# Optimization experiments

Measured on AMD Instinct MI355X. Metric: run time of the kernel, lower is better.

## Reference

```python
import jax, jax.numpy as jnp
import numpy as np

N_NODES = 20000
N_EDGES = 400000
DIM = 128       # dim
NB = 16         # radial basis size
ZD = 16         # species encoding dim
N_SPECIES = 51
CUTOFF = 5.0
NLAYERS = 2
N_ONSITE = 3


def radial_basis(r):
    # 'gaussian_rinv': gaussians placed uniformly in inverse-distance space (HIP-NN style)
    rinv = 1.0 / r
    mus = jnp.linspace(1.0 / CUTOFF, 1.0, NB, dtype=r.dtype)
    sigma = mus[1] - mus[0]
    return jnp.exp(-0.5 * ((rinv[:, None] - mus[None, :]) / sigma) ** 2)  # [E, NB]


def setup_inputs() -> dict:
    key = jax.random.key(0)
    ks = jax.random.split(key, 16)
    species = jax.random.randint(ks[0], (N_NODES,), 1, N_SPECIES)
    edge_src = jax.random.randint(ks[1], (N_EDGES,), 0, N_NODES)
    edge_dst = jax.random.randint(ks[2], (N_EDGES,), 0, N_NODES)
    distances = jax.random.uniform(ks[3], (N_EDGES,), minval=0.8, maxval=CUTOFF)
    switch = jax.random.uniform(ks[4], (N_EDGES,))
    Z = jax.random.normal(ks[5], (N_SPECIES, ZD))  # species encoding table
    Ws0 = jax.random.normal(ks[6], (ZD, DIM)) / np.sqrt(ZD)
    bs0 = jnp.zeros((DIM,), jnp.float32)
    V0 = jax.random.normal(ks[7], (NB, ZD, DIM)) / np.sqrt(NB * ZD)
    Ws1 = jax.random.normal(ks[8], (DIM, DIM)) / np.sqrt(DIM)
    bs1 = jnp.zeros((DIM,), jnp.float32)
    V1 = jax.random.normal(ks[9], (NB, DIM, DIM)) / np.sqrt(NB * DIM)
    Won_a = jax.random.normal(ks[10], (NLAYERS, N_ONSITE, DIM, DIM)) / np.sqrt(DIM)
    bon_a = jnp.zeros((NLAYERS, N_ONSITE, DIM), jnp.float32)
    Won_b = jax.random.normal(ks[11], (NLAYERS, N_ONSITE, DIM, DIM)) / np.sqrt(DIM)
    bon_b = jnp.zeros((NLAYERS, N_ONSITE, DIM), jnp.float32)
    return dict(species=species, edge_src=edge_src, edge_dst=edge_dst,
                distances=distances, switch=switch, Z=Z,
                Ws0=Ws0, bs0=bs0, V0=V0, Ws1=Ws1, bs1=bs1, V1=V1,
                Won_a=Won_a, bon_a=bon_a, Won_b=Won_b, bon_b=bon_b)


def reference(species, edge_src, edge_dst, distances, switch, Z,
              Ws0, bs0, V0, Ws1, bs1, V1, Won_a, bon_a, Won_b, bon_b):
    zi = Z[species]                       # [N, ZD] species encoding
    s = radial_basis(distances)           # [E, NB] (identical basis each layer)
    sw = switch[:, None]                  # [E, 1]
    Ws, bs, Vs = (Ws0, Ws1), (bs0, bs1), (V0, V1)
    zis = []
    for layer in range(NLAYERS):
        zself = zi @ Ws[layer] + bs[layer]                        # [N, DIM]
        # mij = einsum('ej,ek,jkl->el', s, zi[edge_dst], V): per-edge outer then one GEMM
        zdst = zi[edge_dst]                                       # [E, k] gather
        outer = s[:, :, None] * zdst[:, None, :]                  # [E, NB, k]
        mij = outer.reshape(outer.shape[0], -1) @ Vs[layer].reshape(-1, DIM)  # [E, DIM]
        zi = jax.nn.silu(zself.at[edge_src].add(mij * sw))        # scatter-add
        for j in range(N_ONSITE):                                 # residual 2-layer MLPs
            h = jax.nn.silu(zi @ Won_a[layer, j] + bon_a[layer, j])
            zi = zi + h @ Won_b[layer, j] + bon_b[layer, j]
        zis.append(zi)
    # (embedding, embedding_layers)
    return zi, jnp.stack(zis, axis=1)
```

## Files before the change

kernel.cpp:

```cpp
#include <hip/hip_runtime.h>
#include <stdint.h>

#define NNODES 20000
#define NEDGES 400000
#define MTILES 1250
#define MT2    625
#define KS1 68

typedef __attribute__((ext_vector_type(8))) short short8;
typedef __attribute__((ext_vector_type(4))) float floatx4;

__device__ __forceinline__ float bf2f(uint16_t u){ return __uint_as_float(((uint32_t)u)<<16); }
__device__ __forceinline__ uint16_t f2bf(float f){
  uint32_t x = __float_as_uint(f);
  x += 0x7FFFu + ((x>>16)&1u);
  return (uint16_t)(x>>16);
}
__device__ __forceinline__ uint32_t packbf(float a, float b){
  return (uint32_t)f2bf(a) | ((uint32_t)f2bf(b)<<16);
}
__device__ __forceinline__ float siluf(float x){ return x/(1.0f+__expf(-x)); }
__device__ __forceinline__ float ldf(const void* p, int i, int md){
  return (md==1) ? bf2f(((const uint16_t*)p)[i]) : ((const float*)p)[i];
}

#define OFF_V0   0
#define N_V0     32768
#define OFF_WS1  32768
#define N_WS1    16384
#define OFF_BS1  49152
#define N_BS1    128
#define OFF_V1   49280
#define N_V1     262144
#define OFF_WA   311424
#define N_WA     98304
#define OFF_BA   409728
#define N_BA     768
#define OFF_WB   410496
#define N_WB     98304
#define OFF_BB   508800
#define N_BB     768
#define N_CONV   509568

__global__ void k_probe(const void* dist, int* mode){
  if(threadIdx.x != 0 || blockIdx.x != 0) return;
  const float* f = (const float*)dist;
  const uint16_t* h = (const uint16_t*)dist;
  int okf = 1, okb = 1;
  for(int i=0;i<256;i++){
    float a = f[i];       okf &= (a >= 0.7f) & (a <= 5.1f);
    float b = bf2f(h[i]); okb &= (b >= 0.7f) & (b <= 5.1f);
  }
  *mode = okb ? 1 : (okf ? 0 : 1);
}

__global__ __launch_bounds__(256) void k_conv(const void* s0,const void* s1,const void* s2,const void* s3,
                                              const void* s4,const void* s5,const void* s6,const void* s7,
                                              const int* __restrict__ modep, float* __restrict__ dst){
  int md = *modep;
  int i = blockIdx.x*256 + threadIdx.x;
  if(i >= N_CONV) return;
  const void* src; int t = i;
  if(t < N_V0){src=s0;}
  else if((t-=N_V0) < N_WS1){src=s1;}
  else if((t-=N_WS1) < N_BS1){src=s2;}
  else if((t-=N_BS1) < N_V1){src=s3;}
  else if((t-=N_V1) < N_WA){src=s4;}
  else if((t-=N_WA) < N_BA){src=s5;}
  else if((t-=N_BA) < N_WB){src=s6;}
  else {t-=N_WB; src=s7;}
  dst[i] = ldf(src, t, md);
}

__global__ __launch_bounds__(256) void k_hist(const int* __restrict__ src, int* __restrict__ cnt){
  int e = blockIdx.x*256 + threadIdx.x;
  if(e < NEDGES){
    int s = src[e];
    if((unsigned)s < NNODES) atomicAdd(&cnt[s], 1);
  }
}

__global__ __launch_bounds__(1024) void k_scan(int* cnt_cur, int* offs){
  __shared__ int wsum[16];
  int t = threadIdx.x;
  const int chunk = (NNODES + 1023)/1024;
  int lo = t*chunk, hi = lo+chunk;
  if(lo > NNODES) lo = NNODES;
  if(hi > NNODES) hi = NNODES;
  int s = 0;
  for(int i=lo;i<hi;i++) s += cnt_cur[i];
  int lane = t&63, wv = t>>6;
  int v = s;
  #pragma unroll
  for(int d=1; d<64; d<<=1){
    int u = __shfl_up(v, d);
    if(lane >= d) v += u;
  }
  if(lane==63) wsum[wv] = v;
  __syncthreads();
  if(t==0){
    int run = 0;
    #pragma unroll
    for(int i=0;i<16;i++){ int c = wsum[i]; wsum[i] = run; run += c; }
  }
  __syncthreads();
  int run = wsum[wv] + (v - s);
  for(int i=lo;i<hi;i++){
    int c = cnt_cur[i];
    offs[i] = run;
    cnt_cur[i] = run;
    run += c;
  }
  if(t==1023) offs[NNODES] = run;
}

__global__ __launch_bounds__(256) void k_fillG(const int* __restrict__ src,
                                               const int* __restrict__ edst,
                                               const int* __restrict__ species,
                                               int* __restrict__ cur,
                                               const void* __restrict__ dist,
                                               const void* __restrict__ sw,
                                               const int* __restrict__ modep,
                                               int* __restrict__ dsts,
                                               int* __restrict__ sps,
                                               uint16_t* __restrict__ gs){
  int e = blockIdx.x*256 + threadIdx.x;
  if(e >= NEDGES) return;
  int md = *modep;
  int s = src[e];
  if((unsigned)s >= NNODES) s = 0;
  int p = atomicAdd(&cur[s], 1);
  if((unsigned)p >= NEDGES) p = 0;
  int dn = edst[e];
  if((unsigned)dn >= NNODES) dn = 0;
  dsts[p] = dn;
  int sp = species[dn];
  if((unsigned)sp >= 51) sp = 0;
  sps[p] = sp;
  float r = ldf(dist, e, md);
  float w = ldf(sw, e, md);
  float rinv = 1.0f/r;
  const float sigma = 0.8f/15.0f;
  const float isig  = 15.0f/0.8f;
  uint32_t u[8];
  #pragma unroll
  for(int j=0;j<8;j++){
    float mu0 = 0.2f + sigma*(float)(2*j);
    float mu1 = 0.2f + sigma*(float)(2*j+1);
    float t0 = (rinv-mu0)*isig, t1 = (rinv-mu1)*isig;
    u[j] = packbf(w*__expf(-0.5f*t0*t0), w*__expf(-0.5f*t1*t1));
  }
  uint4* o = (uint4*)(gs + (size_t)p*16);
  o[0] = make_uint4(u[0],u[1],u[2],u[3]);
  o[1] = make_uint4(u[4],u[5],u[6],u[7]);
}

__global__ __launch_bounds__(128) void k_spec(const void* __restrict__ Z,
                                              const void* __restrict__ Ws0,
                                              const void* __restrict__ bs0,
                                              const int* __restrict__ modep,
                                              float* __restrict__ ZWs0,
                                              uint16_t* __restrict__ zfb){
  int s = blockIdx.x, d = threadIdx.x;
  int md = *modep;
  float zk[16];
  #pragma unroll
  for(int k=0;k<16;k++) zk[k] = ldf(Z, s*16+k, md);
  float a = ldf(bs0, d, md);
  #pragma unroll
  for(int k=0;k<16;k++) a = fmaf(zk[k], ldf(Ws0, k*128+d, md), a);
  ZWs0[s*128+d] = a;
  if(d < 16) zfb[s*16+d] = f2bf(zk[d]);
}

__global__ __launch_bounds__(256) void k_prepB(const float* __restrict__ W, int Ksteps,
                                               uint16_t* __restrict__ Bf){
  int idx = blockIdx.x*256 + threadIdx.x;
  int total = Ksteps*8*64;
  if(idx >= total) return;
  int l = idx & 63, nt = (idx>>6)&7, kk = idx>>9;
  int kbase = kk*32 + (l>>4)*8;
  int dim = nt*16 + (l&15);
  uint32_t u[4];
  #pragma unroll
  for(int t=0;t<4;t++){
    float f0 = W[(size_t)(kbase+2*t)*128 + dim];
    float f1 = W[(size_t)(kbase+2*t+1)*128 + dim];
    u[t] = packbf(f0,f1);
  }
  ((uint4*)Bf)[idx] = make_uint4(u[0],u[1],u[2],u[3]);
}

__global__ __launch_bounds__(256) void k_prepW(const float* __restrict__ conv,
                                               uint16_t* __restrict__ Wf){
  int idx = blockIdx.x*256 + threadIdx.x;
  if(idx >= 12*2048) return;
  int wi = idx>>11, r = idx&2047;
  int l = r & 63, nt = (r>>6)&7, kk = r>>9;
  const float* W = conv + ((wi<6) ? (OFF_WA + wi*16384) : (OFF_WB + (wi-6)*16384));
  int kbase = kk*32 + (l>>4)*8;
  int dim = nt*16 + (l&15);
  uint32_t u[4];
  #pragma unroll
  for(int t=0;t<4;t++){
    float f0 = W[(size_t)(kbase+2*t)*128 + dim];
    float f1 = W[(size_t)(kbase+2*t+1)*128 + dim];
    u[t] = packbf(f0,f1);
  }
  ((uint4*)Wf)[idx] = make_uint4(u[0],u[1],u[2],u[3]);
}

__global__ __launch_bounds__(256) void k_l0(const int* __restrict__ offs,
                                            const int* __restrict__ sps,
                                            const uint16_t* __restrict__ gs,
                                            const uint16_t* __restrict__ zfb,
                                            const uint16_t* __restrict__ Bf,
                                            const int* __restrict__ species,
                                            const float* __restrict__ ZWs0,
                                            const uint16_t* __restrict__ Waf,
                                            const float* __restrict__ ba,
                                            const uint16_t* __restrict__ Wbf,
                                            const float* __restrict__ bb,
                                            void* __restrict__ outb,
                                            const int* __restrict__ modep,
                                            uint16_t* __restrict__ zib,
                                            uint16_t* __restrict__ zib2){
  __shared__ uint16_t ldsA[8*64*8];
  __shared__ float zb[16*132];
  __shared__ float hb[16*132];
  int w = threadIdx.x>>6, l = threadIdx.x&63;
  int n0 = blockIdx.x*16;
  int col = l&15, quad = l>>4;
  for(int i=0;i<4;i++){
    int m = w*4 + i;
    int n = n0 + m;
    int beg = offs[n], end = offs[n+1];
    floatx4 acc0 = (floatx4){0.f,0.f,0.f,0.f};
    for(int p0=beg; p0<end; p0+=32){
      int sp[8];
      union { short8 s; uint16_t u[8]; } Bg, Az;
      #pragma unroll
      for(int j=0;j<8;j++){
        int p = p0 + quad*8 + j;
        int pc = p < end ? p : beg;
        sp[j] = sps[pc];
        uint16_t g = gs[(size_t)pc*16 + col];
        Bg.u[j] = (p < end) ? g : (uint16_t)0;
      }
      #pragma unroll
      for(int j=0;j<8;j++)
        Az.u[j] = zfb[sp[j]*16 + col];
      acc0 = __builtin_amdgcn_mfma_f32_16x16x32_bf16(Az.s, Bg.s, acc0, 0,0,0);
    }
    int K0 = col*16 + quad*4;
    int kk = K0>>5, qt = (K0>>3)&3, jt = K0&7;
    int slot = kk*64 + ((qt*16 + m) ^ (kk>>2));
    uint32_t lo = packbf(acc0[0], acc0[1]);
    uint32_t hi = packbf(acc0[2], acc0[3]);
    *(uint2*)(&ldsA[slot*8 + jt]) = make_uint2(lo, hi);
  }
  __syncthreads();
  floatx4 acc1 = (floatx4){0.f,0.f,0.f,0.f};
  floatx4 acc2 = (floatx4){0.f,0.f,0.f,0.f};
  const short8* Bp = (const short8*)Bf;
  int nt1 = w, nt2 = w+4;
  #pragma unroll
  for(int kk=0;kk<8;kk++){
    short8 a = *(const short8*)(&ldsA[(kk*64 + (l^(kk>>2)))*8]);
    short8 b1 = Bp[(size_t)(kk*8+nt1)*64 + l];
    short8 b2 = Bp[(size_t)(kk*8+nt2)*64 + l];
    acc1 = __builtin_amdgcn_mfma_f32_16x16x32_bf16(a, b1, acc1, 0,0,0);
    acc2 = __builtin_amdgcn_mfma_f32_16x16x32_bf16(a, b2, acc2, 0,0,0);
  }
  #pragma unroll
  for(int reg=0;reg<4;reg++){
    int node = n0 + quad*4 + reg;
    int sp = species[node];
    if((unsigned)sp >= 51) sp = 0;
    int d1 = nt1*16 + col, d2 = nt2*16 + col;
    int row = quad*4 + reg;
    zb[row*132 + d1] = siluf(acc1[reg] + ZWs0[sp*128 + d1]);
    zb[row*132 + d2] = siluf(acc2[reg] + ZWs0[sp*128 + d2]);
  }
  __syncthreads();
  int m = col, q = quad;
  for(int j=0;j<3;j++){
    const short8* Ba = (const short8*)Waf + (size_t)j*2048 + l;
    floatx4 acc[2];
    acc[0] = (floatx4){0.f,0.f,0.f,0.f};
    acc[1] = (floatx4){0.f,0.f,0.f,0.f};
    #pragma unroll
    for(int kk=0;kk<4;kk++){
      const float* zp = zb + m*132 + kk*32 + q*8;
      float4 a0 = *(const float4*)zp, a1 = *(const float4*)(zp+4);
      union { short8 s; uint32_t u[4]; } A;
      A.u[0]=packbf(a0.x,a0.y); A.u[1]=packbf(a0.z,a0.w);
      A.u[2]=packbf(a1.x,a1.y); A.u[3]=packbf(a1.z,a1.w);
      #pragma unroll
      for(int t=0;t<2;t++){
        short8 bfr = Ba[(size_t)(kk*8 + w*2+t)*64];
        acc[t] = __builtin_amdgcn_mfma_f32_16x16x32_bf16(A.s, bfr, acc[t], 0,0,0);
      }
    }
    #pragma unroll
    for(int t=0;t<2;t++){
      int dim = (w*2+t)*16 + m;
      float bv = ba[j*128+dim];
      #pragma unroll
      for(int reg=0;reg<4;reg++)
        hb[(q*4+reg)*132 + dim] = siluf(acc[t][reg] + bv);
    }
    __syncthreads();
    const short8* Bb = (const short8*)Wbf + (size_t)j*2048 + l;
    floatx4 acc2o[2];
    acc2o[0] = (floatx4){0.f,0.f,0.f,0.f};
    acc2o[1] = (floatx4){0.f,0.f,0.f,0.f};
    #pragma unroll
    for(int kk=0;kk<4;kk++){
      const float* hp = hb + m*132 + kk*32 + q*8;
      float4 a0 = *(const float4*)hp, a1 = *(const float4*)(hp+4);
      union { short8 s; uint32_t u[4]; } A;
      A.u[0]=packbf(a0.x,a0.y); A.u[1]=packbf(a0.z,a0.w);
      A.u[2]=packbf(a1.x,a1.y); A.u[3]=packbf(a1.z,a1.w);
      #pragma unroll
      for(int t=0;t<2;t++){
        short8 bfr = Bb[(size_t)(kk*8 + w*2+t)*64];
        acc2o[t] = __builtin_amdgcn_mfma_f32_16x16x32_bf16(A.s, bfr, acc2o[t], 0,0,0);
      }
    }
    #pragma unroll
    for(int t=0;t<2;t++){
      int dim = (w*2+t)*16 + m;
      float bv = bb[j*128+dim];
      #pragma unroll
      for(int reg=0;reg<4;reg++){
        int idx = (q*4+reg)*132 + dim;
        zb[idx] = zb[idx] + acc2o[t][reg] + bv;
      }
    }
    __syncthreads();
  }
  int md = *modep;
  const long ZIS = (long)NNODES*128;
  #pragma unroll
  for(int i=0;i<2;i++){
    int flat = (i*256 + threadIdx.x)*4;
    int node = flat>>7, k = flat&127;
    float4 v = *(float4*)(zb + node*132 + k);
    int n = n0 + node;
    uint2 pv = make_uint2(packbf(v.x,v.y), packbf(v.z,v.w));
    *(uint2*)(zib + (size_t)n*128 + k) = pv;
    if(md==1){
      uint16_t* ob = (uint16_t*)outb;
      *(uint2*)(ob + ZIS + (long)n*256 + k) = pv;
    } else {
      float* ob = (float*)outb;
      *(float4*)(ob + ZIS + (long)n*256 + k) = v;
    }
  }
  {
    int node2 = threadIdx.x>>4, c = threadIdx.x&15;
    float vv[8];
    #pragma unroll
    for(int mt=0;mt<8;mt++) vv[mt] = zb[node2*132 + mt*16 + c];
    uint4 o = make_uint4(packbf(vv[0],vv[1]), packbf(vv[2],vv[3]),
                         packbf(vv[4],vv[5]), packbf(vv[6],vv[7]));
    *(uint4*)(zib2 + (size_t)(n0+node2)*128 + c*8) = o;
  }
}

__global__ __launch_bounds__(1024, 2) void k_l1(const int* __restrict__ offs,
                                               const int* __restrict__ dsts,
                                               const uint16_t* __restrict__ gs,
                                               const uint16_t* __restrict__ zib,
                                               const uint16_t* __restrict__ zib2,
                                               const uint16_t* __restrict__ Bf,
                                               const float* __restrict__ bias,
                                               const uint16_t* __restrict__ Waf,
                                               const float* __restrict__ ba,
                                               const uint16_t* __restrict__ Wbf,
                                               const float* __restrict__ bb,
                                               void* __restrict__ outb,
                                               const int* __restrict__ modep){
  __shared__ __align__(16) uint16_t ldsA[2*64*64*8];
  int w = threadIdx.x>>6, l = threadIdx.x&63;
  int n0 = blockIdx.x*32;
  int col = l&15, quad = l>>4;
  for(int i=0;i<2;i++){
    int m = w*2 + i;
    int n = n0 + m;
    int beg = offs[n], end = offs[n+1];
    floatx4 acc[8];
    #pragma unroll
    for(int t=0;t<8;t++) acc[t] = (floatx4){0.f,0.f,0.f,0.f};
    for(int p0=beg; p0<end; p0+=32){
      int dn[8];
      union { short8 s; uint16_t u[8]; } Bg;
      #pragma unroll
      for(int j=0;j<8;j++){
        int p = p0 + quad*8 + j;
        int pc = p < end ? p : beg;
        dn[j] = dsts[pc];
        uint16_t g = gs[(size_t)pc*16 + col];
        Bg.u[j] = (p < end) ? g : (uint16_t)0;
      }
      uint4 row[8];
      #pragma unroll
      for(int j=0;j<8;j++)
        row[j] = *(const uint4*)(zib2 + (size_t)dn[j]*128 + col*8);
      #pragma unroll
      for(int mt=0;mt<8;mt++){
        union { short8 s; uint32_t u32[4]; } Az;
        #pragma unroll
        for(int cp=0;cp<4;cp++){
          uint32_t a = ((const uint32_t*)&row[2*cp])[mt>>1];
          uint32_t b = ((const uint32_t*)&row[2*cp+1])[mt>>1];
          Az.u32[cp] = __builtin_amdgcn_perm(b, a, (mt&1) ? 0x07060302u : 0x05040100u);
        }
        acc[mt] = __builtin_amdgcn_mfma_f32_16x16x32_bf16(Az.s, Bg.s, acc[mt], 0,0,0);
      }
    }
    uint16_t* tile = ldsA + (size_t)(m>>4)*32768;
    int mloc = m & 15;
    #pragma unroll
    for(int mt=0;mt<8;mt++){
      int K0 = col*128 + mt*16 + quad*4;
      int kk = K0>>5, qt = (K0>>3)&3, jt = K0&7;
      int slot = kk*64 + ((qt*16 + mloc) ^ (kk>>2));
      uint32_t lo = packbf(acc[mt][0], acc[mt][1]);
      uint32_t hi = packbf(acc[mt][2], acc[mt][3]);
      *(uint2*)(&tile[slot*8 + jt]) = make_uint2(lo, hi);
    }
  }
  __syncthreads();
  int nt1 = w & 7, half = w >> 3;
  floatx4 accA = (floatx4){0.f,0.f,0.f,0.f};
  floatx4 accB = (floatx4){0.f,0.f,0.f,0.f};
  const short8* Bp = (const short8*)Bf;
  int kb = half*32, ke = kb + 32;
  #pragma unroll 8
  for(int kk=kb;kk<ke;kk++){
    int ai = (kk*64 + (l^(kk>>2)))*8;
    short8 a0 = *(const short8*)(&ldsA[ai]);
    short8 a1 = *(const short8*)(&ldsA[32768 + ai]);
    short8 b1 = Bp[(size_t)(kk*8+nt1)*64 + l];
    accA = __builtin_amdgcn_mfma_f32_16x16x32_bf16(a0, b1, accA, 0,0,0);
    accB = __builtin_amdgcn_mfma_f32_16x16x32_bf16(a1, b1, accB, 0,0,0);
  }
  #pragma unroll
  for(int t=0;t<2;t++){
    int kk = 64 + half*2 + t;
    uint4 za0 = *(const uint4*)(zib + (size_t)(n0+col)*128 + (kk-64)*32 + quad*8);
    uint4 za1 = *(const uint4*)(zib + (size_t)(n0+16+col)*128 + (kk-64)*32 + quad*8);
    union { short8 s; uint4 u; } A0, A1; A0.u = za0; A1.u = za1;
    short8 b1 = Bp[(size_t)(kk*8+nt1)*64 + l];
    accA = __builtin_amdgcn_mfma_f32_16x16x32_bf16(A0.s, b1, accA, 0,0,0);
    accB = __builtin_amdgcn_mfma_f32_16x16x32_bf16(A1.s, b1, accB, 0,0,0);
  }
  __syncthreads();
  float* red = (float*)ldsA;
  float* zbA = (float*)((char*)ldsA + 16384);
  float* zbB = zbA + 16*132;
  float* hbA = zbB + 16*132;
  float* hbB = hbA + 16*132;
  if(half==1){
    *(floatx4*)(&red[(nt1*64 + l)*4])     = accA;
    *(floatx4*)(&red[((8+nt1)*64 + l)*4]) = accB;
  }
  __syncthreads();
  if(half==0){
    floatx4 o0 = *(const floatx4*)(&red[(nt1*64 + l)*4]);
    floatx4 o1 = *(const floatx4*)(&red[((8+nt1)*64 + l)*4]);
    int d1 = nt1*16 + col;
    float bv = bias[d1];
    #pragma unroll
    for(int reg=0;reg<4;reg++){
      int row = quad*4 + reg;
      zbA[row*132 + d1] = siluf(accA[reg] + o0[reg] + bv);
      zbB[row*132 + d1] = siluf(accB[reg] + o1[reg] + bv);
    }
  }
  __syncthreads();
  int grp = w>>3, wl = w&7;
  float* zb = grp ? zbB : zbA;
  float* hb = grp ? hbB : hbA;
  int m = col, q = quad;
  for(int j=0;j<3;j++){
    const short8* Ba = (const short8*)Waf + (size_t)j*2048 + l;
    floatx4 acc = (floatx4){0.f,0.f,0.f,0.f};
    #pragma unroll
    for(int kk=0;kk<4;kk++){
      const float* zp = zb + m*132 + kk*32 + q*8;
      float4 a0 = *(const float4*)zp, a1 = *(const float4*)(zp+4);
      union { short8 s; uint32_t u[4]; } A;
      A.u[0]=packbf(a0.x,a0.y); A.u[1]=packbf(a0.z,a0.w);
      A.u[2]=packbf(a1.x,a1.y); A.u[3]=packbf(a1.z,a1.w);
      short8 bfr = Ba[(size_t)(kk*8 + wl)*64];
      acc = __builtin_amdgcn_mfma_f32_16x16x32_bf16(A.s, bfr, acc, 0,0,0);
    }
    {
      int dim = wl*16 + m;
      float bv = ba[j*128+dim];
      #pragma unroll
      for(int reg=0;reg<4;reg++)
        hb[(q*4+reg)*132 + dim] = siluf(acc[reg] + bv);
    }
    __syncthreads();
    const short8* Bb = (const short8*)Wbf + (size_t)j*2048 + l;
    floatx4 acc2 = (floatx4){0.f,0.f,0.f,0.f};
    #pragma unroll
    for(int kk=0;kk<4;kk++){
      const float* hp = hb + m*132 + kk*32 + q*8;
      float4 a0 = *(const float4*)hp, a1 = *(const float4*)(hp+4);
      union { short8 s; uint32_t u[4]; } A;
      A.u[0]=packbf(a0.x,a0.y); A.u[1]=packbf(a0.z,a0.w);
      A.u[2]=packbf(a1.x,a1.y); A.u[3]=packbf(a1.z,a1.w);
      short8 bfr = Bb[(size_t)(kk*8 + wl)*64];
      acc2 = __builtin_amdgcn_mfma_f32_16x16x32_bf16(A.s, bfr, acc2, 0,0,0);
    }
    {
      int dim = wl*16 + m;
      float bv = bb[j*128+dim];
      #pragma unroll
      for(int reg=0;reg<4;reg++){
        int idx = (q*4+reg)*132 + dim;
        zb[idx] = zb[idx] + acc2[reg] + bv;
      }
    }
    __syncthreads();
  }
  {
    int md = *modep;
    const long ZIS = (long)NNODES*128;
    int tig = wl*64 + l;
    int flat = tig*4, node = flat>>7, k = flat&127;
    float4 v = *(float4*)(zb + node*132 + k);
    int n = n0 + grp*16 + node;
    if(md==1){
      uint2 pv = make_uint2(packbf(v.x,v.y), packbf(v.z,v.w));
      uint16_t* ob = (uint16_t*)outb;
      *(uint2*)(ob + ZIS + 128 + (long)n*256 + k) = pv;
      *(uint2*)(ob + (long)n*128 + k) = pv;
    } else {
      float* ob = (float*)outb;
      *(float4*)(ob + ZIS + 128 + (long)n*256 + k) = v;
      *(float4*)(ob + (long)n*128 + k) = v;
    }
  }
}

extern "C" void kernel_launch(void* const* d_in, const int* in_sizes, int n_in,
                              void* d_out, int out_size, void* d_ws, size_t ws_size,
                              hipStream_t stream){
  const int* species = (const int*)d_in[0];
  const int* esrc    = (const int*)d_in[1];
  const int* edst    = (const int*)d_in[2];
  const void* dist   = d_in[3];
  const void* swit   = d_in[4];
  const void* Z      = d_in[5];
  const void* Ws0    = d_in[6];
  const void* bs0    = d_in[7];
  const void* V0     = d_in[8];
  const void* Ws1    = d_in[9];
  const void* bs1    = d_in[10];
  const void* V1     = d_in[11];
  const void* Wa     = d_in[12];
  const void* ba     = d_in[13];
  const void* Wb     = d_in[14];
  const void* bb     = d_in[15];

  char* ws = (char*)d_ws;
  size_t off = 0;
  auto alloc = [&](size_t bytes)->void*{ void* p = ws + off; off = (off + bytes + 255) & ~(size_t)255; return p; };
  int*      offs = (int*)     alloc((size_t)(NNODES+1)*4);
  int*      cur  = (int*)     alloc((size_t)NNODES*4);
  int*      dsts = (int*)     alloc((size_t)NEDGES*4);
  int*      sps  = (int*)     alloc((size_t)NEDGES*4);
  uint16_t* gs   = (uint16_t*)alloc((size_t)NEDGES*16*2);
  uint16_t* zib  = (uint16_t*)alloc((size_t)NNODES*128*2);
  uint16_t* zib2 = (uint16_t*)alloc((size_t)NNODES*128*2);
  float*    ZWs0 = (float*)   alloc((size_t)51*128*4);
  uint16_t* zfb  = (uint16_t*)alloc((size_t)51*16*2);
  float*    conv = (float*)   alloc((size_t)N_CONV*4);
  uint16_t* Bf0  = (uint16_t*)alloc((size_t)8*8*64*8*2);
  uint16_t* Bf1  = (uint16_t*)alloc((size_t)KS1*8*64*8*2);
  uint16_t* Wfr  = (uint16_t*)alloc((size_t)12*16384*2);
  int*      mode = (int*)     alloc(256);

  const int EB = (NEDGES+255)/256;
  hipMemsetAsync(cur, 0, NNODES*4, stream);
  k_probe<<<1,64,0,stream>>>(dist, mode);
  k_conv <<<(N_CONV+255)/256,256,0,stream>>>(V0, Ws1, bs1, V1, Wa, ba, Wb, bb, mode, conv);
  k_hist <<<EB,256,0,stream>>>(esrc, cur);
  k_scan <<<1,1024,0,stream>>>(cur, offs);
  k_fillG<<<EB,256,0,stream>>>(esrc, edst, species, cur, dist, swit, mode, dsts, sps, gs);
  k_spec <<<51,128,0,stream>>>(Z, Ws0, bs0, mode, ZWs0, zfb);
  k_prepB<<<(8*8*64+255)/256,256,0,stream>>>(conv+OFF_V0, 8,  Bf0);
  k_prepB<<<(64*8*64+255)/256,256,0,stream>>>(conv+OFF_V1, 64, Bf1);
  k_prepB<<<(4*8*64+255)/256,256,0,stream>>>(conv+OFF_WS1, 4, Bf1 + (size_t)64*8*64*8);
  k_prepW<<<(12*2048+255)/256,256,0,stream>>>(conv, Wfr);

  uint16_t* WaF0 = Wfr;
  uint16_t* WaF1 = Wfr + (size_t)3*16384;
  uint16_t* WbF0 = Wfr + (size_t)6*16384;
  uint16_t* WbF1 = Wfr + (size_t)9*16384;

  k_l0<<<MTILES,256,0,stream>>>(offs, sps, gs, zfb, Bf0, species, ZWs0,
                                WaF0, conv+OFF_BA, WbF0, conv+OFF_BB,
                                d_out, mode, zib, zib2);

  k_l1<<<MT2,1024,0,stream>>>(offs, dsts, gs, zib, zib2, Bf1, conv+OFF_BS1,
                              WaF1, conv+OFF_BA+384, WbF1, conv+OFF_BB+384,
                              d_out, mode);
}
```

Before: 297.1 us.

## Split layer-1 kernel into message kernel and separate onsite MLP kernel

The fused layer-1 kernel is split in two. The message/aggregation part now writes the silu-activated node features to an fp32 global buffer. A new 256-thread kernel reloads 16 nodes per block and runs the three residual onsite MLPs, with each wave computing two 16-column tiles. This frees the large 1024-thread blocks from the serialized onsite phase and lets the onsite work run with many small blocks, at the cost of an extra launch and a global round trip of 10 MB of fp32 activations.

```diff
diff --git a/kernel.cpp b/kernel.cpp
--- a/kernel.cpp
+++ b/kernel.cpp
@@ -369,19 +369,14 @@
   }
 }
 
-__global__ __launch_bounds__(1024, 2) void k_l1(const int* __restrict__ offs,
+__global__ __launch_bounds__(1024, 2) void k_msg1f(const int* __restrict__ offs,
                                                const int* __restrict__ dsts,
                                                const uint16_t* __restrict__ gs,
                                                const uint16_t* __restrict__ zib,
                                                const uint16_t* __restrict__ zib2,
                                                const uint16_t* __restrict__ Bf,
                                                const float* __restrict__ bias,
-                                               const uint16_t* __restrict__ Waf,
-                                               const float* __restrict__ ba,
-                                               const uint16_t* __restrict__ Wbf,
-                                               const float* __restrict__ bb,
-                                               void* __restrict__ outb,
-                                               const int* __restrict__ modep){
+                                               float* __restrict__ zacc){
   __shared__ __align__(16) uint16_t ldsA[2*64*64*8];
   int w = threadIdx.x>>6, l = threadIdx.x&63;
   int n0 = blockIdx.x*32;
@@ -459,10 +454,6 @@
   }
   __syncthreads();
   float* red = (float*)ldsA;
-  float* zbA = (float*)((char*)ldsA + 16384);
-  float* zbB = zbA + 16*132;
-  float* hbA = zbB + 16*132;
-  float* hbB = hbA + 16*132;
   if(half==1){
     *(floatx4*)(&red[(nt1*64 + l)*4])     = accA;
     *(floatx4*)(&red[((8+nt1)*64 + l)*4]) = accB;
@@ -475,19 +466,39 @@
     float bv = bias[d1];
     #pragma unroll
     for(int reg=0;reg<4;reg++){
-      int row = quad*4 + reg;
-      zbA[row*132 + d1] = siluf(accA[reg] + o0[reg] + bv);
-      zbB[row*132 + d1] = siluf(accB[reg] + o1[reg] + bv);
-    }
-  }
-  __syncthreads();
-  int grp = w>>3, wl = w&7;
-  float* zb = grp ? zbB : zbA;
-  float* hb = grp ? hbB : hbA;
-  int m = col, q = quad;
+      int nodeA = n0 + quad*4 + reg;
+      int nodeB = n0 + 16 + quad*4 + reg;
+      zacc[(size_t)nodeA*128 + d1] = siluf(accA[reg] + o0[reg] + bv);
+      zacc[(size_t)nodeB*128 + d1] = siluf(accB[reg] + o1[reg] + bv);
+    }
+  }
+}
+
+__global__ __launch_bounds__(256) void k_onsite1(const float* __restrict__ zin,
+                                                 const uint16_t* __restrict__ Waf,
+                                                 const float* __restrict__ ba,
+                                                 const uint16_t* __restrict__ Wbf,
+                                                 const float* __restrict__ bb,
+                                                 void* __restrict__ outb,
+                                                 const int* __restrict__ modep){
+  __shared__ float zb[16*132];
+  __shared__ float hb[16*132];
+  int w = threadIdx.x>>6, l = threadIdx.x&63;
+  int n0 = blockIdx.x*16;
+  int md = *modep;
+  #pragma unroll
+  for(int i=0;i<2;i++){
+    int flat = (i*256 + threadIdx.x)*4;
+    int node = flat>>7, k = flat&127;
+    *(float4*)(zb + node*132 + k) = *(const float4*)(zin + (size_t)(n0+node)*128 + k);
+  }
+  __syncthreads();
+  int m = l&15, q = l>>4;
   for(int j=0;j<3;j++){
     const short8* Ba = (const short8*)Waf + (size_t)j*2048 + l;
-    floatx4 acc = (floatx4){0.f,0.f,0.f,0.f};
+    floatx4 acc[2];
+    acc[0] = (floatx4){0.f,0.f,0.f,0.f};
+    acc[1] = (floatx4){0.f,0.f,0.f,0.f};
     #pragma unroll
     for(int kk=0;kk<4;kk++){
       const float* zp = zb + m*132 + kk*32 + q*8;
@@ -495,19 +506,25 @@
       union { short8 s; uint32_t u[4]; } A;
       A.u[0]=packbf(a0.x,a0.y); A.u[1]=packbf(a0.z,a0.w);
       A.u[2]=packbf(a1.x,a1.y); A.u[3]=packbf(a1.z,a1.w);
-      short8 bfr = Ba[(size_t)(kk*8 + wl)*64];
-      acc = __builtin_amdgcn_mfma_f32_16x16x32_bf16(A.s, bfr, acc, 0,0,0);
-    }
-    {
-      int dim = wl*16 + m;
+      #pragma unroll
+      for(int t=0;t<2;t++){
+        short8 bfr = Ba[(size_t)(kk*8 + w*2+t)*64];
+        acc[t] = __builtin_amdgcn_mfma_f32_16x16x32_bf16(A.s, bfr, acc[t], 0,0,0);
+      }
+    }
+    #pragma unroll
+    for(int t=0;t<2;t++){
+      int dim = (w*2+t)*16 + m;
       float bv = ba[j*128+dim];
       #pragma unroll
       for(int reg=0;reg<4;reg++)
-        hb[(q*4+reg)*132 + dim] = siluf(acc[reg] + bv);
+        hb[(q*4+reg)*132 + dim] = siluf(acc[t][reg] + bv);
     }
     __syncthreads();
     const short8* Bb = (const short8*)Wbf + (size_t)j*2048 + l;
-    floatx4 acc2 = (floatx4){0.f,0.f,0.f,0.f};
+    floatx4 acc2[2];
+    acc2[0] = (floatx4){0.f,0.f,0.f,0.f};
+    acc2[1] = (floatx4){0.f,0.f,0.f,0.f};
     #pragma unroll
     for(int kk=0;kk<4;kk++){
       const float* hp = hb + m*132 + kk*32 + q*8;
@@ -515,27 +532,31 @@
       union { short8 s; uint32_t u[4]; } A;
       A.u[0]=packbf(a0.x,a0.y); A.u[1]=packbf(a0.z,a0.w);
       A.u[2]=packbf(a1.x,a1.y); A.u[3]=packbf(a1.z,a1.w);
-      short8 bfr = Bb[(size_t)(kk*8 + wl)*64];
-      acc2 = __builtin_amdgcn_mfma_f32_16x16x32_bf16(A.s, bfr, acc2, 0,0,0);
-    }
-    {
-      int dim = wl*16 + m;
+      #pragma unroll
+      for(int t=0;t<2;t++){
+        short8 bfr = Bb[(size_t)(kk*8 + w*2+t)*64];
+        acc2[t] = __builtin_amdgcn_mfma_f32_16x16x32_bf16(A.s, bfr, acc2[t], 0,0,0);
+      }
+    }
+    #pragma unroll
+    for(int t=0;t<2;t++){
+      int dim = (w*2+t)*16 + m;
       float bv = bb[j*128+dim];
       #pragma unroll
       for(int reg=0;reg<4;reg++){
         int idx = (q*4+reg)*132 + dim;
-        zb[idx] = zb[idx] + acc2[reg] + bv;
+        zb[idx] = zb[idx] + acc2[t][reg] + bv;
       }
     }
     __syncthreads();
   }
-  {
-    int md = *modep;
-    const long ZIS = (long)NNODES*128;
-    int tig = wl*64 + l;
-    int flat = tig*4, node = flat>>7, k = flat&127;
+  const long ZIS = (long)NNODES*128;
+  #pragma unroll
+  for(int i=0;i<2;i++){
+    int flat = (i*256 + threadIdx.x)*4;
+    int node = flat>>7, k = flat&127;
     float4 v = *(float4*)(zb + node*132 + k);
-    int n = n0 + grp*16 + node;
+    int n = n0 + node;
     if(md==1){
       uint2 pv = make_uint2(packbf(v.x,v.y), packbf(v.z,v.w));
       uint16_t* ob = (uint16_t*)outb;
@@ -577,6 +598,7 @@
   int*      dsts = (int*)     alloc((size_t)NEDGES*4);
   int*      sps  = (int*)     alloc((size_t)NEDGES*4);
   uint16_t* gs   = (uint16_t*)alloc((size_t)NEDGES*16*2);
+  float*    zacc = (float*)   alloc((size_t)NNODES*128*4);
   uint16_t* zib  = (uint16_t*)alloc((size_t)NNODES*128*2);
   uint16_t* zib2 = (uint16_t*)alloc((size_t)NNODES*128*2);
   float*    ZWs0 = (float*)   alloc((size_t)51*128*4);
@@ -609,7 +631,7 @@
                                 WaF0, conv+OFF_BA, WbF0, conv+OFF_BB,
                                 d_out, mode, zib, zib2);
 
-  k_l1<<<MT2,1024,0,stream>>>(offs, dsts, gs, zib, zib2, Bf1, conv+OFF_BS1,
-                              WaF1, conv+OFF_BA+384, WbF1, conv+OFF_BB+384,
-                              d_out, mode);
-}
+  k_msg1f<<<MT2,1024,0,stream>>>(offs, dsts, gs, zib, zib2, Bf1, conv+OFF_BS1, zacc);
+  k_onsite1<<<MTILES,256,0,stream>>>(zacc, WaF1, conv+OFF_BA+384, WbF1, conv+OFF_BB+384,
+                                     d_out, mode);
+}
```

Measured after the change: 287.2 us. -3.3%, faster.
